# Performance work log

Hardware: AMD Instinct MI355X
Metric: run time of the kernel (lower is better)

The kernel has to match this reference:

```python
import jax, jax.numpy as jnp
import numpy as np

ALPHA = 0.25
GAMMA = 2.0
VAR0, VAR1 = 0.1, 0.2  # torch.Tensor([0.1, 0.2]) variances in encode
EPS = 1e-4


def _center_size(boxes):
    # corner (x1,y1,x2,y2) -> center (cx,cy,w,h)
    return jnp.concatenate([(boxes[:, :2] + boxes[:, 2:]) * 0.5,
                            boxes[:, 2:] - boxes[:, :2]], axis=1)


def _jaccard(a, b):
    # a: [A,4] anchors, b: [T,4] targets, corner form -> IoU [A,T]
    lt = jnp.maximum(a[:, None, :2], b[None, :, :2])
    rb = jnp.minimum(a[:, None, 2:], b[None, :, 2:])
    wh = jnp.clip(rb - lt, 0.0)
    inter = wh[..., 0] * wh[..., 1]
    area_a = (a[:, 2] - a[:, 0]) * (a[:, 3] - a[:, 1])
    area_b = (b[:, 2] - b[:, 0]) * (b[:, 3] - b[:, 1])
    return inter / (area_a[:, None] + area_b[None, :] - inter)


def _encode(matched, priors_cf):
    # matched: corner form [P,4]; priors_cf: center form [P,4]
    g_cxcy = ((matched[:, :2] + matched[:, 2:]) * 0.5 - priors_cf[:, :2]) / (VAR0 * priors_cf[:, 2:])
    g_wh = jnp.log((matched[:, 2:] - matched[:, :2]) / priors_cf[:, 2:]) / VAR1
    return jnp.concatenate([g_cxcy, g_wh], axis=1)


def _per_image(cla, reg, target, anchor, anchor_cf):
    # cla [A,C], reg [A,4], target [T,5]
    valid = target[:, 4] != -1.0                      # padded targets (label -1) are excluded
    has_valid = jnp.any(valid)
    cla = jnp.clip(cla, EPS, 1.0 - EPS)
    iou = _jaccard(anchor, target[:, :4])             # [A,T]
    iou = jnp.where(valid[None, :], iou, -1.0)        # mask padded targets (valid IoUs are >= 0)
    iou_argmax = jnp.argmax(iou, axis=1)              # [A]
    iou_max = jnp.take_along_axis(iou, iou_argmax[:, None], axis=1)[:, 0]
    pos = iou_max >= 0.5
    num_pos = jnp.sum(pos)
    assigned = target[iou_argmax]                     # [A,5] gather of matched gt

    C = cla.shape[1]
    onehot = jax.nn.one_hot(assigned[:, 4].astype(jnp.int32), C, dtype=cla.dtype)
    labels = jnp.full_like(cla, -1.0)
    labels = jnp.where(iou_max[:, None] < 0.4, 0.0, labels)
    labels = jnp.where(pos[:, None], onehot, labels)

    is_one = labels == 1.0
    alpha_factor = jnp.where(is_one, ALPHA, 1.0 - ALPHA)
    focal_weight = alpha_factor * jnp.where(is_one, 1.0 - cla, cla) ** GAMMA
    bce = -(labels * jnp.log(cla) + (1.0 - labels) * jnp.log1p(-cla))
    cls_loss = jnp.where(labels != -1.0, focal_weight * bce, 0.0)
    cls_loss = cls_loss.sum() / jnp.maximum(num_pos.astype(cla.dtype), 1.0)

    # smooth-L1 on positive anchors only; original takes .mean() over [P,4]
    enc_gt = _encode(assigned[:, :4], anchor_cf)      # [A,4]
    diff = jnp.abs(enc_gt - reg)
    sl1 = jnp.where(diff <= 1.0 / 9.0, 0.5 * 9.0 * diff * diff, diff - 0.5 / 9.0)
    denom = jnp.maximum(num_pos * 4, 1).astype(cla.dtype)
    reg_loss = jnp.where(num_pos > 0, jnp.sum(sl1 * pos[:, None]) / denom, 0.0)

    cls_loss = jnp.where(has_valid, cls_loss, 0.0)
    reg_loss = jnp.where(has_valid, reg_loss, 0.0)
    return cls_loss, reg_loss


def setup_inputs() -> dict:
    key = jax.random.key(0)
    ks = jax.random.split(key, 7)
    B, A, C, T = 8, 100000, 80, 50
    clas = jax.random.uniform(ks[0], (B, A, C), jnp.float32, 0.01, 0.99)
    regs = jax.random.normal(ks[1], (B, A, 4), jnp.float32)
    # anchors: valid corner boxes inside a ~1024x1024 image
    axy = jax.random.uniform(ks[2], (1, A, 2), jnp.float32, 0.0, 900.0)
    awh = jax.random.uniform(ks[3], (1, A, 2), jnp.float32, 16.0, 120.0)
    anchors = jnp.concatenate([axy, axy + awh], axis=-1)
    # targets: valid gt boxes with class id in [0, C) stored as float in column 4
    txy = jax.random.uniform(ks[4], (B, T, 2), jnp.float32, 0.0, 800.0)
    twh = jax.random.uniform(ks[5], (B, T, 2), jnp.float32, 20.0, 220.0)
    lab = jax.random.randint(ks[6], (B, T, 1), 0, C).astype(jnp.float32)
    targets = jnp.concatenate([txy, txy + twh, lab], axis=-1)
    return {"clas": clas, "regs": regs, "anchors": anchors, "targets": targets}


def reference(clas, regs, anchors, targets):
    anchor = anchors[0]                               # [A,4]
    anchor_cf = _center_size(anchor)
    cls_l, reg_l = jax.vmap(_per_image, in_axes=(0, 0, 0, None, None))(
        clas, regs, targets, anchor, anchor_cf)
    return (jnp.mean(cls_l, keepdims=True), jnp.mean(reg_l, keepdims=True))
```

## Files before the change

### kernel.cpp

```cpp
#include <hip/hip_runtime.h>

#define A_COUNT 100000
#define B_COUNT 8
#define C_COUNT 80
#define T_COUNT 50
#define BLOCK   256
#define NF4     (C_COUNT / 4)

typedef float f4v __attribute__((ext_vector_type(4)));

__global__ __launch_bounds__(BLOCK) void retina_main(
    const float* __restrict__ clas,
    const float* __restrict__ regs,
    const float* __restrict__ anchors,
    const float* __restrict__ targets,
    float* __restrict__ ws_cls,
    float* __restrict__ ws_reg,
    int*   __restrict__ ws_pos)
{
    __shared__ int   s_state[BLOCK];
    __shared__ float s_c[4], s_r[4];
    __shared__ int   s_p[4];

    const int b    = blockIdx.y;
    const int base = blockIdx.x * BLOCK;
    const int tid  = threadIdx.x;
    const int a    = base + tid;
    const int nA   = min(BLOCK, A_COUNT - base);
    const bool full = (nA == BLOCK);

    const f4v* cl4 = (const f4v*)(clas + ((size_t)b * A_COUNT + base) * C_COUNT);

    f4v buf[8];
    if (full) {
        #pragma unroll
        for (int u = 0; u < 6; ++u)
            buf[u] = __builtin_nontemporal_load(&cl4[tid + u * BLOCK]);
    }

    const float* tgt = targets + b * T_COUNT * 5;

    const int ac = min(a, A_COUNT - 1);
    const float4 an = ((const float4*)anchors)[ac];
    const float area_a = (an.z - an.x) * (an.w - an.y);

    float best = -1.0f;
    int   bestIdx = 0;
    bool  anyValid = false;

    #pragma unroll 5
    for (int t = 0; t < T_COUNT; ++t) {
        const float tx1 = tgt[t * 5 + 0];
        const float ty1 = tgt[t * 5 + 1];
        const float tx2 = tgt[t * 5 + 2];
        const float ty2 = tgt[t * 5 + 3];
        const float lab = tgt[t * 5 + 4];
        const bool valid = (lab != -1.0f);
        anyValid |= valid;
        const float lx = fmaxf(an.x, tx1), ly = fmaxf(an.y, ty1);
        const float rx = fminf(an.z, tx2), ry = fminf(an.w, ty2);
        const float w = fmaxf(rx - lx, 0.0f);
        const float h = fmaxf(ry - ly, 0.0f);
        const float inter  = w * h;
        const float area_b = (tx2 - tx1) * (ty2 - ty1);
        const float denom  = area_a + area_b - inter;
        float iou = inter * __builtin_amdgcn_rcpf(denom);
        iou = valid ? iou : -1.0f;
        if (iou > best) { best = iou; bestIdx = t; }
    }

    int   state  = -1;
    float my_reg = 0.0f;
    bool  my_pos = false;

    if (a < A_COUNT && anyValid) {
        if (best >= 0.5f) {
            const float tx1 = tgt[bestIdx * 5 + 0];
            const float ty1 = tgt[bestIdx * 5 + 1];
            const float tx2 = tgt[bestIdx * 5 + 2];
            const float ty2 = tgt[bestIdx * 5 + 3];
            state  = (int)tgt[bestIdx * 5 + 4];
            my_pos = true;
            const float4 rg = ((const float4*)regs)[(size_t)b * A_COUNT + a];
            const float pcx = (an.x + an.z) * 0.5f, pcy = (an.y + an.w) * 0.5f;
            const float pw  = an.z - an.x,          ph  = an.w - an.y;
            const float mcx = (tx1 + tx2) * 0.5f,   mcy = (ty1 + ty2) * 0.5f;
            const float mw  = tx2 - tx1,            mh  = ty2 - ty1;
            const float e0 = (mcx - pcx) / (0.1f * pw);
            const float e1 = (mcy - pcy) / (0.1f * ph);
            const float e2 = __logf(mw / pw) * 5.0f;
            const float e3 = __logf(mh / ph) * 5.0f;
            const float d0 = fabsf(e0 - rg.x);
            const float d1 = fabsf(e1 - rg.y);
            const float d2 = fabsf(e2 - rg.z);
            const float d3 = fabsf(e3 - rg.w);
            const float th = 1.0f / 9.0f;
            const float c59 = 0.5f / 9.0f;
            const float s0 = (d0 <= th) ? 4.5f * d0 * d0 : d0 - c59;
            const float s1 = (d1 <= th) ? 4.5f * d1 * d1 : d1 - c59;
            const float s2 = (d2 <= th) ? 4.5f * d2 * d2 : d2 - c59;
            const float s3 = (d3 <= th) ? 4.5f * d3 * d3 : d3 - c59;
            my_reg = s0 + s1 + s2 + s3;
        } else if (best < 0.4f) {
            state = 128;
        }
    }
    s_state[tid] = state;
    __syncthreads();

    float cls2 = 0.0f;

    if (full) {
        int aL = tid / NF4;
        int cL = tid - aL * NF4;
        #pragma unroll
        for (int i = 0; i < 20; ++i) {
            if (i + 6 < 20)
                buf[(i + 6) & 7] = __builtin_nontemporal_load(&cl4[tid + (i + 6) * BLOCK]);
            const f4v v = buf[i & 7];
            const int st = s_state[aL];
            float sum4 = 0.0f;
            #pragma unroll
            for (int j = 0; j < 4; ++j) {
                const float p  = v[j];
                const float l2 = __builtin_amdgcn_logf(1.0f - p);
                sum4 = fmaf(p * p, l2, sum4);
            }
            cls2 += (st == -1) ? 0.0f : sum4;
            aL += 12; cL += 16;
            if (cL >= NF4) { cL -= NF4; ++aL; }
        }
    } else {
        const int count4 = nA * NF4;
        for (int i = tid; i < count4; i += BLOCK) {
            const int st = s_state[i / NF4];
            if (st == -1) continue;
            const f4v v = __builtin_nontemporal_load(&cl4[i]);
            float sum4 = 0.0f;
            #pragma unroll
            for (int j = 0; j < 4; ++j) {
                const float p  = v[j];
                const float l2 = __builtin_amdgcn_logf(1.0f - p);
                sum4 = fmaf(p * p, l2, sum4);
            }
            cls2 += sum4;
        }
    }

    float cls_local = cls2 * (-0.75f * 0.69314718056f);

    if (my_pos) {
        float p = clas[((size_t)b * A_COUNT + a) * C_COUNT + state];
        p = fminf(fmaxf(p, 1e-4f), 1.0f - 1e-4f);
        const float om = 1.0f - p;
        cls_local += 0.25f * om * om * (-__logf(p))
                   - 0.75f * p * p * (-__logf(om));
    }

    float r0 = cls_local, r1 = my_reg;
    const unsigned long long bal = __ballot(my_pos);
    const int posc = __popcll(bal);
    #pragma unroll
    for (int off = 32; off > 0; off >>= 1) {
        r0 += __shfl_down(r0, off);
        r1 += __shfl_down(r1, off);
    }
    const int wave = tid >> 6, lane = tid & 63;
    if (lane == 0) { s_c[wave] = r0; s_r[wave] = r1; s_p[wave] = posc; }
    __syncthreads();
    if (tid == 0) {
        float tc = 0.0f, tr = 0.0f; int tp = 0;
        #pragma unroll
        for (int w = 0; w < 4; ++w) { tc += s_c[w]; tr += s_r[w]; tp += s_p[w]; }
        atomicAdd(&ws_cls[b], tc);
        atomicAdd(&ws_reg[b], tr);
        atomicAdd(&ws_pos[b], tp);
    }
}

__global__ void retina_final(const float* __restrict__ ws_cls,
                             const float* __restrict__ ws_reg,
                             const int*   __restrict__ ws_pos,
                             float* __restrict__ out)
{
    const int tid = threadIdx.x;
    float cl = 0.0f, rl = 0.0f;
    if (tid < B_COUNT) {
        const int   npi = ws_pos[tid];
        const float np  = (float)npi;
        cl = ws_cls[tid] / fmaxf(np, 1.0f);
        rl = (npi > 0) ? ws_reg[tid] / (np * 4.0f) : 0.0f;
    }
    #pragma unroll
    for (int off = 4; off > 0; off >>= 1) {
        cl += __shfl_down(cl, off);
        rl += __shfl_down(rl, off);
    }
    if (tid == 0) {
        out[0] = cl * (1.0f / (float)B_COUNT);
        out[1] = rl * (1.0f / (float)B_COUNT);
    }
}

extern "C" void kernel_launch(void* const* d_in, const int* in_sizes, int n_in,
                              void* d_out, int out_size, void* d_ws, size_t ws_size,
                              hipStream_t stream) {
    const float* clas    = (const float*)d_in[0];
    const float* regs    = (const float*)d_in[1];
    const float* anchors = (const float*)d_in[2];
    const float* targets = (const float*)d_in[3];

    float* ws_cls = (float*)d_ws;
    float* ws_reg = ws_cls + B_COUNT;
    int*   ws_pos = (int*)(ws_reg + B_COUNT);

    hipMemsetAsync(d_ws, 0, (2 * B_COUNT) * sizeof(float) + B_COUNT * sizeof(int), stream);

    dim3 grid((A_COUNT + BLOCK - 1) / BLOCK, B_COUNT);
    retina_main<<<grid, BLOCK, 0, stream>>>(clas, regs, anchors, targets,
                                            ws_cls, ws_reg, ws_pos);
    retina_final<<<1, 64, 0, stream>>>(ws_cls, ws_reg, ws_pos, (float*)d_out);
}
```

Measured before the change: 390.5 us.

## Split fused kernel into anchor-matching pass and streaming classification sweep

Splits the single fused kernel into two. The first computes IoU matching, the regression loss and the positive-class correction, and writes a per-anchor keep bitmask to the workspace. The second streams the class-probability tensor with a deeper 8-deep load buffer and weights each anchor's sum by the mask. The aim is a lean, high-occupancy streaming kernel that no longer waits on matching before it starts loading. The cost is an extra launch, a global bitmask round trip, and no overlap of the matching compute with the loads.

Measured after the change: 434.0 us. 11.1% more time.

```diff
diff --git a/kernel.cpp b/kernel.cpp
--- a/kernel.cpp
+++ b/kernel.cpp
@@ -6,19 +6,20 @@
 #define T_COUNT 50
 #define BLOCK   256
 #define NF4     (C_COUNT / 4)
+#define KWORDS  ((A_COUNT + 63) / 64)
 
 typedef float f4v __attribute__((ext_vector_type(4)));
 
-__global__ __launch_bounds__(BLOCK) void retina_main(
+__global__ __launch_bounds__(BLOCK) void retina_match(
     const float* __restrict__ clas,
     const float* __restrict__ regs,
     const float* __restrict__ anchors,
     const float* __restrict__ targets,
     float* __restrict__ ws_cls,
     float* __restrict__ ws_reg,
-    int*   __restrict__ ws_pos)
+    int*   __restrict__ ws_pos,
+    unsigned long long* __restrict__ ws_keep)
 {
-    __shared__ int   s_state[BLOCK];
     __shared__ float s_c[4], s_r[4];
     __shared__ int   s_p[4];
 
@@ -26,17 +27,6 @@
     const int base = blockIdx.x * BLOCK;
     const int tid  = threadIdx.x;
     const int a    = base + tid;
-    const int nA   = min(BLOCK, A_COUNT - base);
-    const bool full = (nA == BLOCK);
-
-    const f4v* cl4 = (const f4v*)(clas + ((size_t)b * A_COUNT + base) * C_COUNT);
-
-    f4v buf[8];
-    if (full) {
-        #pragma unroll
-        for (int u = 0; u < 6; ++u)
-            buf[u] = __builtin_nontemporal_load(&cl4[tid + u * BLOCK]);
-    }
 
     const float* tgt = targets + b * T_COUNT * 5;
 
@@ -105,59 +95,24 @@
             state = 128;
         }
     }
-    s_state[tid] = state;
-    __syncthreads();
-
-    float cls2 = 0.0f;
-
-    if (full) {
-        int aL = tid / NF4;
-        int cL = tid - aL * NF4;
-        #pragma unroll
-        for (int i = 0; i < 20; ++i) {
-            if (i + 6 < 20)
-                buf[(i + 6) & 7] = __builtin_nontemporal_load(&cl4[tid + (i + 6) * BLOCK]);
-            const f4v v = buf[i & 7];
-            const int st = s_state[aL];
-            float sum4 = 0.0f;
-            #pragma unroll
-            for (int j = 0; j < 4; ++j) {
-                const float p  = v[j];
-                const float l2 = __builtin_amdgcn_logf(1.0f - p);
-                sum4 = fmaf(p * p, l2, sum4);
-            }
-            cls2 += (st == -1) ? 0.0f : sum4;
-            aL += 12; cL += 16;
-            if (cL >= NF4) { cL -= NF4; ++aL; }
-        }
-    } else {
-        const int count4 = nA * NF4;
-        for (int i = tid; i < count4; i += BLOCK) {
-            const int st = s_state[i / NF4];
-            if (st == -1) continue;
-            const f4v v = __builtin_nontemporal_load(&cl4[i]);
-            float sum4 = 0.0f;
-            #pragma unroll
-            for (int j = 0; j < 4; ++j) {
-                const float p  = v[j];
-                const float l2 = __builtin_amdgcn_logf(1.0f - p);
-                sum4 = fmaf(p * p, l2, sum4);
-            }
-            cls2 += sum4;
-        }
-    }
-
-    float cls_local = cls2 * (-0.75f * 0.69314718056f);
-
+
+    const bool keep = (state != -1);
+    const unsigned long long kb = __ballot(keep);
+    const int wave = tid >> 6, lane = tid & 63;
+    const int widx = blockIdx.x * 4 + wave;
+    if (lane == 0 && widx < KWORDS)
+        ws_keep[(size_t)b * KWORDS + widx] = kb;
+
+    float corr = 0.0f;
     if (my_pos) {
         float p = clas[((size_t)b * A_COUNT + a) * C_COUNT + state];
         p = fminf(fmaxf(p, 1e-4f), 1.0f - 1e-4f);
         const float om = 1.0f - p;
-        cls_local += 0.25f * om * om * (-__logf(p))
-                   - 0.75f * p * p * (-__logf(om));
-    }
-
-    float r0 = cls_local, r1 = my_reg;
+        corr = 0.25f * om * om * (-__logf(p))
+             - 0.75f * p * p * (-__logf(om));
+    }
+
+    float r0 = corr, r1 = my_reg;
     const unsigned long long bal = __ballot(my_pos);
     const int posc = __popcll(bal);
     #pragma unroll
@@ -165,7 +120,6 @@
         r0 += __shfl_down(r0, off);
         r1 += __shfl_down(r1, off);
     }
-    const int wave = tid >> 6, lane = tid & 63;
     if (lane == 0) { s_c[wave] = r0; s_r[wave] = r1; s_p[wave] = posc; }
     __syncthreads();
     if (tid == 0) {
@@ -175,6 +129,80 @@
         atomicAdd(&ws_cls[b], tc);
         atomicAdd(&ws_reg[b], tr);
         atomicAdd(&ws_pos[b], tp);
+    }
+}
+
+__global__ __launch_bounds__(BLOCK) void retina_sweep(
+    const float* __restrict__ clas,
+    const unsigned long long* __restrict__ ws_keep,
+    float* __restrict__ ws_cls)
+{
+    __shared__ float s_w[BLOCK];
+    __shared__ float s_c[4];
+
+    const int b    = blockIdx.y;
+    const int base = blockIdx.x * BLOCK;
+    const int tid  = threadIdx.x;
+    const int nA   = min(BLOCK, A_COUNT - base);
+
+    const int widx = min(blockIdx.x * 4 + (tid >> 6), KWORDS - 1);
+    const unsigned long long kw = ws_keep[(size_t)b * KWORDS + widx];
+    s_w[tid] = ((kw >> (tid & 63)) & 1ULL) ? 1.0f : 0.0f;
+    __syncthreads();
+
+    const f4v* cl4 = (const f4v*)(clas + ((size_t)b * A_COUNT + base) * C_COUNT);
+    float cls2 = 0.0f;
+
+    if (nA == BLOCK) {
+        f4v buf[8];
+        #pragma unroll
+        for (int u = 0; u < 8; ++u)
+            buf[u] = __builtin_nontemporal_load(&cl4[tid + u * BLOCK]);
+        int aL = tid / NF4;
+        int cL = tid - aL * NF4;
+        #pragma unroll
+        for (int i = 0; i < 20; ++i) {
+            const f4v v = buf[i & 7];
+            if (i + 8 < 20)
+                buf[i & 7] = __builtin_nontemporal_load(&cl4[tid + (i + 8) * BLOCK]);
+            const float w = s_w[aL];
+            float sum4 = 0.0f;
+            #pragma unroll
+            for (int j = 0; j < 4; ++j) {
+                const float p  = v[j];
+                const float l2 = __builtin_amdgcn_logf(1.0f - p);
+                sum4 = fmaf(p * p, l2, sum4);
+            }
+            cls2 = fmaf(sum4, w, cls2);
+            aL += 12; cL += 16;
+            if (cL >= NF4) { cL -= NF4; ++aL; }
+        }
+    } else {
+        const int count4 = nA * NF4;
+        for (int i = tid; i < count4; i += BLOCK) {
+            const f4v v = __builtin_nontemporal_load(&cl4[i]);
+            const float w = s_w[i / NF4];
+            float sum4 = 0.0f;
+            #pragma unroll
+            for (int j = 0; j < 4; ++j) {
+                const float p  = v[j];
+                const float l2 = __builtin_amdgcn_logf(1.0f - p);
+                sum4 = fmaf(p * p, l2, sum4);
+            }
+            cls2 = fmaf(sum4, w, cls2);
+        }
+    }
+
+    float r0 = cls2;
+    #pragma unroll
+    for (int off = 32; off > 0; off >>= 1)
+        r0 += __shfl_down(r0, off);
+    const int wave = tid >> 6, lane = tid & 63;
+    if (lane == 0) s_c[wave] = r0;
+    __syncthreads();
+    if (tid == 0) {
+        float tc = s_c[0] + s_c[1] + s_c[2] + s_c[3];
+        atomicAdd(&ws_cls[b], tc * (-0.75f * 0.69314718056f));
     }
 }
 
@@ -213,11 +241,14 @@
     float* ws_cls = (float*)d_ws;
     float* ws_reg = ws_cls + B_COUNT;
     int*   ws_pos = (int*)(ws_reg + B_COUNT);
-
-    hipMemsetAsync(d_ws, 0, (2 * B_COUNT) * sizeof(float) + B_COUNT * sizeof(int), stream);
+    unsigned long long* ws_keep =
+        (unsigned long long*)((char*)d_ws + 96);
+
+    hipMemsetAsync(d_ws, 0, 96, stream);
 
     dim3 grid((A_COUNT + BLOCK - 1) / BLOCK, B_COUNT);
-    retina_main<<<grid, BLOCK, 0, stream>>>(clas, regs, anchors, targets,
-                                            ws_cls, ws_reg, ws_pos);
+    retina_match<<<grid, BLOCK, 0, stream>>>(clas, regs, anchors, targets,
+                                             ws_cls, ws_reg, ws_pos, ws_keep);
+    retina_sweep<<<grid, BLOCK, 0, stream>>>(clas, ws_keep, ws_cls);
     retina_final<<<1, 64, 0, stream>>>(ws_cls, ws_reg, ws_pos, (float*)d_out);
 }
```
